# Kernel tuning notes

Measured on AMD Instinct MI355X. Metric: run time of the kernel, lower is better.

## Reference

```python
import jax, jax.numpy as jnp
import numpy as np

N_NODES = 100000
N_EDGES = 1600000
F_IN = 128
DIM = 64
N_CLASSES = 40


def setup_inputs() -> dict:
    key = jax.random.key(0)
    ks = jax.random.split(key, 12)
    x = jax.random.normal(ks[0], (N_NODES, F_IN), dtype=jnp.float32)
    edge_index = jax.random.randint(ks[1], (2, N_EDGES), 0, N_NODES, dtype=jnp.int64)
    s = lambda fan_in: 1.0 / np.sqrt(fan_in)
    W1 = jax.random.uniform(ks[2], (F_IN, DIM), jnp.float32, -s(F_IN), s(F_IN))
    b1 = jax.random.uniform(ks[3], (DIM,), jnp.float32, -s(F_IN), s(F_IN))
    W2 = jax.random.uniform(ks[4], (DIM, DIM), jnp.float32, -s(DIM), s(DIM))
    b2 = jax.random.uniform(ks[5], (DIM,), jnp.float32, -s(DIM), s(DIM))
    Wf1 = jax.random.uniform(ks[6], (DIM, DIM), jnp.float32, -s(DIM), s(DIM))
    bf1 = jax.random.uniform(ks[7], (DIM,), jnp.float32, -s(DIM), s(DIM))
    Wf2 = jax.random.uniform(ks[8], (DIM, N_CLASSES), jnp.float32, -s(DIM), s(DIM))
    bf2 = jax.random.uniform(ks[9], (N_CLASSES,), jnp.float32, -s(DIM), s(DIM))
    return {"x": x, "edge_index": edge_index, "W1": W1, "b1": b1,
            "W2": W2, "b2": b2, "Wf1": Wf1, "bf1": bf1, "Wf2": Wf2, "bf2": bf2}


def _gin_agg(h, src, dst, n_nodes):
    # sum_{j in N(i)} h_j : gather along src, scatter-add to dst
    return jax.ops.segment_sum(h[src], dst, num_segments=n_nodes)


def reference(x, edge_index, W1, b1, W2, b2, Wf1, bf1, Wf2, bf2):
    src, dst = edge_index[0], edge_index[1]
    n = x.shape[0]
    # GINConv(Linear), eps=0: Linear(x + sum_neighbors)
    h = jax.nn.relu((x + _gin_agg(x, src, dst, n)) @ W1 + b1)
    h = jax.nn.relu((h + _gin_agg(h, src, dst, n)) @ W2 + b2)
    h = jax.nn.relu(h @ Wf1 + bf1)  # dropout p=0.5 is identity at inference
    logits = h @ Wf2 + bf2
    return jax.nn.log_softmax(logits, axis=1)
```

## Files before the change

kernel.cpp:

```cpp
#include <hip/hip_runtime.h>

#define NN 100000
#define NE 1600000
#define F_IN 128
#define DIM 64
#define NC 40
#define NB 196
#define MAXBE 10240

typedef unsigned short ushort_t;
typedef __attribute__((ext_vector_type(8))) short bf16x8;
typedef __attribute__((ext_vector_type(4))) float f32x4;

static __device__ __forceinline__ float b2f(ushort_t u) {
  return __uint_as_float(((unsigned)u) << 16);
}
static __device__ __forceinline__ ushort_t f2b(float f) {
  unsigned x = __float_as_uint(f);
  return (ushort_t)((x + 0x7fffu + ((x >> 16) & 1u)) >> 16);
}
static __device__ __forceinline__ unsigned pack2(float a, float b) {
  return (unsigned)f2b(a) | ((unsigned)f2b(b) << 16);
}

__global__ __launch_bounds__(256) void k_prep(const float* __restrict__ W1,
                                              const float* __restrict__ W2,
                                              const float* __restrict__ Wf1,
                                              const float* __restrict__ Wf2,
                                              ushort_t* __restrict__ W1T,
                                              ushort_t* __restrict__ W2T,
                                              ushort_t* __restrict__ Wf1T,
                                              ushort_t* __restrict__ Wf2T,
                                              int* __restrict__ bcur) {
  int t = threadIdx.x;
  if (t < NB) bcur[t] = 0;
  for (int i = t; i < 64 * 128; i += 256) { int c = i >> 7, k = i & 127; W1T[i] = f2b(W1[k * 64 + c]); }
  for (int i = t; i < 64 * 64; i += 256)  { int c = i >> 6, k = i & 63;  W2T[i] = f2b(W2[k * 64 + c]); }
  for (int i = t; i < 64 * 64; i += 256)  { int c = i >> 6, k = i & 63;  Wf1T[i] = f2b(Wf1[k * 64 + c]); }
  for (int i = t; i < 48 * 64; i += 256)  { int c = i >> 6, k = i & 63;  Wf2T[i] = (c < NC) ? f2b(Wf2[k * NC + c]) : (ushort_t)0; }
}

__global__ __launch_bounds__(256) void k_part(const int* __restrict__ src,
                                              const int* __restrict__ dst,
                                              int* __restrict__ bcur,
                                              unsigned* __restrict__ part) {
  __shared__ int hist[NB];
  __shared__ int gbase[NB];
  int t = threadIdx.x;
  for (int i = t; i < NB; i += 256) hist[i] = 0;
  __syncthreads();
  int e0 = blockIdx.x * 4096;
  int s[16], dd[16], r[16];
#pragma unroll
  for (int i = 0; i < 16; ++i) {
    int e = e0 + i * 256 + t;
    if (e < NE) {
      dd[i] = dst[e];
      s[i] = src[e];
      r[i] = atomicAdd(&hist[dd[i] >> 9], 1);
    }
  }
  __syncthreads();
  for (int i = t; i < NB; i += 256)
    gbase[i] = hist[i] ? atomicAdd(&bcur[i], hist[i]) : 0;
  __syncthreads();
#pragma unroll
  for (int i = 0; i < 16; ++i) {
    int e = e0 + i * 256 + t;
    if (e < NE) {
      int b = dd[i] >> 9;
      part[(size_t)b * MAXBE + gbase[b] + r[i]] = ((unsigned)(dd[i] & 511) << 17) | (unsigned)s[i];
    }
  }
}

__global__ __launch_bounds__(256) void k_csr(const int* __restrict__ bcur,
                                             const unsigned* __restrict__ part,
                                             int* __restrict__ cnt,
                                             int* __restrict__ offs,
                                             int* __restrict__ slots) {
  __shared__ unsigned pb[MAXBE];
  __shared__ ushort_t rk[MAXBE];
  __shared__ int lcnt[512], loff[512];
  int b = blockIdx.x, t = threadIdx.x;
  int start = b * MAXBE;
  int m = bcur[b];
  if (m > MAXBE) m = MAXBE;
  lcnt[t] = 0; lcnt[t + 256] = 0;
  __syncthreads();
  for (int i = t; i < m; i += 256) {
    unsigned v = part[start + i];
    pb[i] = v;
    rk[i] = (ushort_t)atomicAdd(&lcnt[v >> 17], 1);
  }
  __syncthreads();
  int o0 = lcnt[t], o1 = lcnt[t + 256];
  __syncthreads();
  for (int off = 1; off < 512; off <<= 1) {
    int v0 = (t >= off) ? lcnt[t - off] : 0;
    int v1 = (t + 256 >= off) ? lcnt[t + 256 - off] : 0;
    __syncthreads();
    lcnt[t] += v0;
    lcnt[t + 256] += v1;
    __syncthreads();
  }
  loff[t] = lcnt[t] - o0;
  loff[t + 256] = lcnt[t + 256] - o1;
  int node0 = b << 9;
  if (node0 + t < NN)       { cnt[node0 + t] = o0;       offs[node0 + t] = start + loff[t]; }
  if (node0 + t + 256 < NN) { cnt[node0 + t + 256] = o1; offs[node0 + t + 256] = start + loff[t + 256]; }
  __syncthreads();
  for (int i = t; i < m; i += 256) {
    unsigned v = pb[i];
    slots[start + loff[v >> 17] + rk[i]] = (int)(v & 0x1FFFFu);
  }
}

__global__ __launch_bounds__(256) void k_agg(const ushort_t* __restrict__ yb,
                                             const int* __restrict__ cnt,
                                             const int* __restrict__ offs,
                                             const int* __restrict__ slots,
                                             const float* __restrict__ bias,
                                             ushort_t* __restrict__ hb) {
  int wv = threadIdx.x >> 6, l = threadIdx.x & 63;
  int h = l >> 5;
  int n = blockIdx.x * 8 + wv * 2 + h;
  int li = l & 31;
  int g = (l >> 3) & 3;
  int q = l & 7;
  int cb = q * 16;
  int deg = cnt[n], start = offs[n];
  deg = deg > 64 ? 64 : deg;
  int sv0 = (li < deg) ? slots[start + li] : 0;
  int sv1 = (32 + li < deg) ? slots[start + 32 + li] : 0;
  int dego = __shfl_xor(deg, 32);
  int degmax = deg > dego ? deg : dego;
  float acc[8];
#pragma unroll
  for (int i = 0; i < 8; ++i) acc[i] = 0.f;
  const char* ybp = (const char*)yb;
  int hbase = h << 5;
  for (int j = 0; j < degmax; j += 16) {
    int i0 = j + g, i1 = j + 4 + g, i2 = j + 8 + g, i3 = j + 12 + g;
    int sa, sb, sc, sd;
    if (j < 32) {
      sa = __shfl(sv0, hbase + i0); sb = __shfl(sv0, hbase + i1);
      sc = __shfl(sv0, hbase + i2); sd = __shfl(sv0, hbase + i3);
    } else {
      sa = __shfl(sv1, hbase + (i0 & 31)); sb = __shfl(sv1, hbase + (i1 & 31));
      sc = __shfl(sv1, hbase + (i2 & 31)); sd = __shfl(sv1, hbase + (i3 & 31));
    }
    uint4 u0 = {0,0,0,0}, u1 = {0,0,0,0}, u2 = {0,0,0,0}, u3 = {0,0,0,0};
    if (i0 < deg) u0 = *(const uint4*)(ybp + (size_t)sa * 128 + cb);
    if (i1 < deg) u1 = *(const uint4*)(ybp + (size_t)sb * 128 + cb);
    if (i2 < deg) u2 = *(const uint4*)(ybp + (size_t)sc * 128 + cb);
    if (i3 < deg) u3 = *(const uint4*)(ybp + (size_t)sd * 128 + cb);
    acc[0] += __uint_as_float(u0.x << 16);  acc[1] += __uint_as_float(u0.x & 0xffff0000u);
    acc[2] += __uint_as_float(u0.y << 16);  acc[3] += __uint_as_float(u0.y & 0xffff0000u);
    acc[4] += __uint_as_float(u0.z << 16);  acc[5] += __uint_as_float(u0.z & 0xffff0000u);
    acc[6] += __uint_as_float(u0.w << 16);  acc[7] += __uint_as_float(u0.w & 0xffff0000u);
    acc[0] += __uint_as_float(u1.x << 16);  acc[1] += __uint_as_float(u1.x & 0xffff0000u);
    acc[2] += __uint_as_float(u1.y << 16);  acc[3] += __uint_as_float(u1.y & 0xffff0000u);
    acc[4] += __uint_as_float(u1.z << 16);  acc[5] += __uint_as_float(u1.z & 0xffff0000u);
    acc[6] += __uint_as_float(u1.w << 16);  acc[7] += __uint_as_float(u1.w & 0xffff0000u);
    acc[0] += __uint_as_float(u2.x << 16);  acc[1] += __uint_as_float(u2.x & 0xffff0000u);
    acc[2] += __uint_as_float(u2.y << 16);  acc[3] += __uint_as_float(u2.y & 0xffff0000u);
    acc[4] += __uint_as_float(u2.z << 16);  acc[5] += __uint_as_float(u2.z & 0xffff0000u);
    acc[6] += __uint_as_float(u2.w << 16);  acc[7] += __uint_as_float(u2.w & 0xffff0000u);
    acc[0] += __uint_as_float(u3.x << 16);  acc[1] += __uint_as_float(u3.x & 0xffff0000u);
    acc[2] += __uint_as_float(u3.y << 16);  acc[3] += __uint_as_float(u3.y & 0xffff0000u);
    acc[4] += __uint_as_float(u3.z << 16);  acc[5] += __uint_as_float(u3.z & 0xffff0000u);
    acc[6] += __uint_as_float(u3.w << 16);  acc[7] += __uint_as_float(u3.w & 0xffff0000u);
  }
#pragma unroll
  for (int i = 0; i < 8; ++i) {
    acc[i] += __shfl_xor(acc[i], 8);
    acc[i] += __shfl_xor(acc[i], 16);
  }
  if (li < 8) {
    uint4 yr = *(const uint4*)&yb[(size_t)n * 64 + q * 8];
    float4 ba = *(const float4*)&bias[q * 8];
    float4 bb = *(const float4*)&bias[q * 8 + 4];
    float v0 = fmaxf(__uint_as_float(yr.x << 16)         + acc[0] + ba.x, 0.f);
    float v1 = fmaxf(__uint_as_float(yr.x & 0xffff0000u) + acc[1] + ba.y, 0.f);
    float v2 = fmaxf(__uint_as_float(yr.y << 16)         + acc[2] + ba.z, 0.f);
    float v3 = fmaxf(__uint_as_float(yr.y & 0xffff0000u) + acc[3] + ba.w, 0.f);
    float v4 = fmaxf(__uint_as_float(yr.z << 16)         + acc[4] + bb.x, 0.f);
    float v5 = fmaxf(__uint_as_float(yr.z & 0xffff0000u) + acc[5] + bb.y, 0.f);
    float v6 = fmaxf(__uint_as_float(yr.w << 16)         + acc[6] + bb.z, 0.f);
    float v7 = fmaxf(__uint_as_float(yr.w & 0xffff0000u) + acc[7] + bb.w, 0.f);
    uint4 st;
    st.x = pack2(v0, v1);
    st.y = pack2(v2, v3);
    st.z = pack2(v4, v5);
    st.w = pack2(v6, v7);
    *(uint4*)&hb[(size_t)n * 64 + q * 8] = st;
  }
}

__global__ __launch_bounds__(256) void k_gemm1(const float* __restrict__ x,
                                               const ushort_t* __restrict__ W1T,
                                               ushort_t* __restrict__ yb) {
  __shared__ ushort_t H[64 * 136];
  int t = threadIdx.x, w = t >> 6, l = t & 63;
  int g = l >> 4, r16 = l & 15;
  int node0 = blockIdx.x * 64;
  bf16x8 B[4][4];
#pragma unroll
  for (int nt = 0; nt < 4; ++nt)
#pragma unroll
    for (int kt = 0; kt < 4; ++kt)
      B[nt][kt] = *(const bf16x8*)&W1T[(16 * nt + r16) * 128 + 32 * kt + 8 * g];
#pragma unroll
  for (int j = 0; j < 8; ++j) {
    int f = t + 256 * j;
    int e = f * 4;
    int n = e >> 7, c = e & 127;
    int gn = node0 + n; if (gn >= NN) gn = NN - 1;
    float4 v = *(const float4*)&x[(size_t)gn * 128 + c];
    ushort4 pv;
    pv.x = f2b(v.x); pv.y = f2b(v.y); pv.z = f2b(v.z); pv.w = f2b(v.w);
    *(ushort4*)&H[n * 136 + c] = pv;
  }
  __syncthreads();
  f32x4 acc[4] = {{0.f,0.f,0.f,0.f},{0.f,0.f,0.f,0.f},{0.f,0.f,0.f,0.f},{0.f,0.f,0.f,0.f}};
#pragma unroll
  for (int kt = 0; kt < 4; ++kt) {
    bf16x8 A = *(const bf16x8*)&H[(16 * w + r16) * 136 + 32 * kt + 8 * g];
#pragma unroll
    for (int nt = 0; nt < 4; ++nt)
      acc[nt] = __builtin_amdgcn_mfma_f32_16x16x32_bf16(A, B[nt][kt], acc[nt], 0, 0, 0);
  }
#pragma unroll
  for (int nt = 0; nt < 4; ++nt)
#pragma unroll
    for (int i = 0; i < 4; ++i) {
      int node = node0 + 16 * w + 4 * g + i;
      if (node < NN)
        yb[(size_t)node * 64 + 16 * nt + r16] = f2b(acc[nt][i]);
    }
}

__global__ __launch_bounds__(256) void k_mid(const ushort_t* __restrict__ hb,
                                             const ushort_t* __restrict__ W2T,
                                             ushort_t* __restrict__ yb) {
  __shared__ ushort_t H[64 * 72];
  int t = threadIdx.x, w = t >> 6, l = t & 63;
  int g = l >> 4, r16 = l & 15;
  int node0 = blockIdx.x * 64;
  bf16x8 B[4][2];
#pragma unroll
  for (int nt = 0; nt < 4; ++nt)
#pragma unroll
    for (int kt = 0; kt < 2; ++kt)
      B[nt][kt] = *(const bf16x8*)&W2T[(16 * nt + r16) * 64 + 32 * kt + 8 * g];
#pragma unroll
  for (int j = 0; j < 2; ++j) {
    int i = t + 256 * j;
    int n = i >> 3, c8 = (i & 7) * 8;
    int gn = node0 + n; if (gn >= NN) gn = NN - 1;
    uint4 u = *(const uint4*)&hb[(size_t)gn * 64 + c8];
    *(uint4*)&H[n * 72 + c8] = u;
  }
  __syncthreads();
  f32x4 acc[4] = {{0.f,0.f,0.f,0.f},{0.f,0.f,0.f,0.f},{0.f,0.f,0.f,0.f},{0.f,0.f,0.f,0.f}};
#pragma unroll
  for (int kt = 0; kt < 2; ++kt) {
    bf16x8 A = *(const bf16x8*)&H[(16 * w + r16) * 72 + 32 * kt + 8 * g];
#pragma unroll
    for (int nt = 0; nt < 4; ++nt)
      acc[nt] = __builtin_amdgcn_mfma_f32_16x16x32_bf16(A, B[nt][kt], acc[nt], 0, 0, 0);
  }
#pragma unroll
  for (int nt = 0; nt < 4; ++nt)
#pragma unroll
    for (int i = 0; i < 4; ++i) {
      int node = node0 + 16 * w + 4 * g + i;
      if (node < NN)
        yb[(size_t)node * 64 + 16 * nt + r16] = f2b(acc[nt][i]);
    }
}

__global__ __launch_bounds__(256) void k_final(const ushort_t* __restrict__ hb,
                                               const ushort_t* __restrict__ Wf1T,
                                               const float* __restrict__ bf1,
                                               const ushort_t* __restrict__ Wf2T,
                                               const float* __restrict__ bf2,
                                               float* __restrict__ out) {
  __shared__ ushort_t H[64 * 72];
  __shared__ ushort_t H2[64 * 72];
  int t = threadIdx.x, w = t >> 6, l = t & 63;
  int g = l >> 4, r16 = l & 15;
  int node0 = blockIdx.x * 64;
  bf16x8 B1[4][2], B2[3][2];
#pragma unroll
  for (int nt = 0; nt < 4; ++nt)
#pragma unroll
    for (int kt = 0; kt < 2; ++kt)
      B1[nt][kt] = *(const bf16x8*)&Wf1T[(16 * nt + r16) * 64 + 32 * kt + 8 * g];
#pragma unroll
  for (int nt = 0; nt < 3; ++nt)
#pragma unroll
    for (int kt = 0; kt < 2; ++kt)
      B2[nt][kt] = *(const bf16x8*)&Wf2T[(16 * nt + r16) * 64 + 32 * kt + 8 * g];
#pragma unroll
  for (int j = 0; j < 2; ++j) {
    int i = t + 256 * j;
    int n = i >> 3, c8 = (i & 7) * 8;
    int gn = node0 + n; if (gn >= NN) gn = NN - 1;
    uint4 u = *(const uint4*)&hb[(size_t)gn * 64 + c8];
    *(uint4*)&H[n * 72 + c8] = u;
  }
  __syncthreads();
  f32x4 acc[4] = {{0.f,0.f,0.f,0.f},{0.f,0.f,0.f,0.f},{0.f,0.f,0.f,0.f},{0.f,0.f,0.f,0.f}};
#pragma unroll
  for (int kt = 0; kt < 2; ++kt) {
    bf16x8 A = *(const bf16x8*)&H[(16 * w + r16) * 72 + 32 * kt + 8 * g];
#pragma unroll
    for (int nt = 0; nt < 4; ++nt)
      acc[nt] = __builtin_amdgcn_mfma_f32_16x16x32_bf16(A, B1[nt][kt], acc[nt], 0, 0, 0);
  }
#pragma unroll
  for (int nt = 0; nt < 4; ++nt) {
    float bias = bf1[16 * nt + r16];
#pragma unroll
    for (int i = 0; i < 4; ++i) {
      float v = fmaxf(acc[nt][i] + bias, 0.f);
      H2[(16 * w + 4 * g + i) * 72 + 16 * nt + r16] = f2b(v);
    }
  }
  __syncthreads();
  f32x4 acc2[3] = {{0.f,0.f,0.f,0.f},{0.f,0.f,0.f,0.f},{0.f,0.f,0.f,0.f}};
#pragma unroll
  for (int kt = 0; kt < 2; ++kt) {
    bf16x8 A2 = *(const bf16x8*)&H2[(16 * w + r16) * 72 + 32 * kt + 8 * g];
#pragma unroll
    for (int nt = 0; nt < 3; ++nt)
      acc2[nt] = __builtin_amdgcn_mfma_f32_16x16x32_bf16(A2, B2[nt][kt], acc2[nt], 0, 0, 0);
  }
  float lg[3][4];
#pragma unroll
  for (int nt = 0; nt < 3; ++nt) {
    int col = 16 * nt + r16;
    float bias = (col < NC) ? bf2[col] : 0.f;
#pragma unroll
    for (int i = 0; i < 4; ++i)
      lg[nt][i] = (col < NC) ? acc2[nt][i] + bias : -1e30f;
  }
#pragma unroll
  for (int i = 0; i < 4; ++i) {
    float m = fmaxf(fmaxf(lg[0][i], lg[1][i]), lg[2][i]);
#pragma unroll
    for (int off = 1; off < 16; off <<= 1) m = fmaxf(m, __shfl_xor(m, off));
    float s = 0.f;
#pragma unroll
    for (int nt = 0; nt < 3; ++nt)
      s += (lg[nt][i] > -1e29f) ? __expf(lg[nt][i] - m) : 0.f;
#pragma unroll
    for (int off = 1; off < 16; off <<= 1) s += __shfl_xor(s, off);
    float ls = __logf(s);
    int node = node0 + 16 * w + 4 * g + i;
#pragma unroll
    for (int nt = 0; nt < 3; ++nt) {
      int col = 16 * nt + r16;
      if (col < NC && node < NN)
        out[(size_t)node * NC + col] = lg[nt][i] - m - ls;
    }
  }
}

extern "C" void kernel_launch(void* const* d_in, const int* in_sizes, int n_in,
                              void* d_out, int out_size, void* d_ws, size_t ws_size,
                              hipStream_t stream) {
  const float* x   = (const float*)d_in[0];
  const int*   ei  = (const int*)d_in[1];
  const float* W1  = (const float*)d_in[2];
  const float* b1  = (const float*)d_in[3];
  const float* W2  = (const float*)d_in[4];
  const float* b2  = (const float*)d_in[5];
  const float* Wf1 = (const float*)d_in[6];
  const float* bf1 = (const float*)d_in[7];
  const float* Wf2 = (const float*)d_in[8];
  const float* bf2 = (const float*)d_in[9];
  float* out = (float*)d_out;

  char* ws = (char*)d_ws;
  size_t o = 0;
  int* bcur  = (int*)(ws + o); o += 4096;
  int* cnt   = (int*)(ws + o); o += 400000;
  int* offs  = (int*)(ws + o); o += 400000;
  o = (o + 255) & ~(size_t)255;
  ushort_t* W1T  = (ushort_t*)(ws + o); o += 64 * 128 * 2;
  ushort_t* W2T  = (ushort_t*)(ws + o); o += 64 * 64 * 2;
  ushort_t* Wf1T = (ushort_t*)(ws + o); o += 64 * 64 * 2;
  ushort_t* Wf2T = (ushort_t*)(ws + o); o += 48 * 64 * 2;
  o = (o + 255) & ~(size_t)255;
  unsigned* part = (unsigned*)(ws + o); o += (size_t)NB * MAXBE * 4;
  int* slots = (int*)(ws + o); o += (size_t)NB * MAXBE * 4;
  ushort_t* yb = (ushort_t*)(ws + o); o += (size_t)NN * DIM * 2;
  ushort_t* hb = (ushort_t*)(ws + o); o += (size_t)NN * DIM * 2;

  const int* srcp = ei;
  const int* dstp = ei + NE;

  k_prep<<<1, 256, 0, stream>>>(W1, W2, Wf1, Wf2, W1T, W2T, Wf1T, Wf2T, bcur);
  k_part<<<(NE + 4095) / 4096, 256, 0, stream>>>(srcp, dstp, bcur, part);
  k_csr<<<NB, 256, 0, stream>>>(bcur, part, cnt, offs, slots);
  k_gemm1<<<(NN + 63) / 64, 256, 0, stream>>>(x, W1T, yb);
  k_agg<<<NN / 8, 256, 0, stream>>>(yb, cnt, offs, slots, b1, hb);
  k_mid<<<(NN + 63) / 64, 256, 0, stream>>>(hb, W2T, yb);
  k_agg<<<NN / 8, 256, 0, stream>>>(yb, cnt, offs, slots, b2, hb);
  k_final<<<(NN + 63) / 64, 256, 0, stream>>>(hb, Wf1T, bf1, Wf2T, bf2, out);
}
```

Baseline: 168.4 us.

## Fuse neighbor aggregation into the following GEMM kernels via shared memory

```diff
diff --git a/kernel.cpp b/kernel.cpp
--- a/kernel.cpp
+++ b/kernel.cpp
@@ -116,20 +116,60 @@
   }
 }
 
-__global__ __launch_bounds__(256) void k_agg(const ushort_t* __restrict__ yb,
-                                             const int* __restrict__ cnt,
-                                             const int* __restrict__ offs,
-                                             const int* __restrict__ slots,
-                                             const float* __restrict__ bias,
-                                             ushort_t* __restrict__ hb) {
-  int wv = threadIdx.x >> 6, l = threadIdx.x & 63;
-  int h = l >> 5;
-  int n = blockIdx.x * 8 + wv * 2 + h;
-  int li = l & 31;
-  int g = (l >> 3) & 3;
-  int q = l & 7;
+__global__ __launch_bounds__(256) void k_gemm1(const float* __restrict__ x,
+                                               const ushort_t* __restrict__ W1T,
+                                               ushort_t* __restrict__ yb) {
+  __shared__ ushort_t H[64 * 136];
+  int t = threadIdx.x, w = t >> 6, l = t & 63;
+  int g = l >> 4, r16 = l & 15;
+  int node0 = blockIdx.x * 64;
+  bf16x8 B[4][4];
+#pragma unroll
+  for (int nt = 0; nt < 4; ++nt)
+#pragma unroll
+    for (int kt = 0; kt < 4; ++kt)
+      B[nt][kt] = *(const bf16x8*)&W1T[(16 * nt + r16) * 128 + 32 * kt + 8 * g];
+#pragma unroll
+  for (int j = 0; j < 8; ++j) {
+    int f = t + 256 * j;
+    int e = f * 4;
+    int n = e >> 7, c = e & 127;
+    int gn = node0 + n; if (gn >= NN) gn = NN - 1;
+    float4 v = *(const float4*)&x[(size_t)gn * 128 + c];
+    ushort4 pv;
+    pv.x = f2b(v.x); pv.y = f2b(v.y); pv.z = f2b(v.z); pv.w = f2b(v.w);
+    *(ushort4*)&H[n * 136 + c] = pv;
+  }
+  __syncthreads();
+  f32x4 acc[4] = {{0.f,0.f,0.f,0.f},{0.f,0.f,0.f,0.f},{0.f,0.f,0.f,0.f},{0.f,0.f,0.f,0.f}};
+#pragma unroll
+  for (int kt = 0; kt < 4; ++kt) {
+    bf16x8 A = *(const bf16x8*)&H[(16 * w + r16) * 136 + 32 * kt + 8 * g];
+#pragma unroll
+    for (int nt = 0; nt < 4; ++nt)
+      acc[nt] = __builtin_amdgcn_mfma_f32_16x16x32_bf16(A, B[nt][kt], acc[nt], 0, 0, 0);
+  }
+#pragma unroll
+  for (int nt = 0; nt < 4; ++nt)
+#pragma unroll
+    for (int i = 0; i < 4; ++i) {
+      int node = node0 + 16 * w + 4 * g + i;
+      if (node < NN)
+        yb[(size_t)node * 64 + 16 * nt + r16] = f2b(acc[nt][i]);
+    }
+}
+
+static __device__ __forceinline__ void agg_round(const ushort_t* __restrict__ yb,
+                                                 const int* __restrict__ cnt,
+                                                 const int* __restrict__ offs,
+                                                 const int* __restrict__ slots,
+                                                 const float* __restrict__ bias,
+                                                 ushort_t* __restrict__ H,
+                                                 int n, int nl,
+                                                 int li, int ag, int q, int h) {
   int cb = q * 16;
-  int deg = cnt[n], start = offs[n];
+  int deg = 0, start = 0;
+  if (n < NN) { deg = cnt[n]; start = offs[n]; }
   deg = deg > 64 ? 64 : deg;
   int sv0 = (li < deg) ? slots[start + li] : 0;
   int sv1 = (32 + li < deg) ? slots[start + 32 + li] : 0;
@@ -141,7 +181,7 @@
   const char* ybp = (const char*)yb;
   int hbase = h << 5;
   for (int j = 0; j < degmax; j += 16) {
-    int i0 = j + g, i1 = j + 4 + g, i2 = j + 8 + g, i3 = j + 12 + g;
+    int i0 = j + ag, i1 = j + 4 + ag, i2 = j + 8 + ag, i3 = j + 12 + ag;
     int sa, sb, sc, sd;
     if (j < 32) {
       sa = __shfl(sv0, hbase + i0); sb = __shfl(sv0, hbase + i1);
@@ -177,7 +217,7 @@
     acc[i] += __shfl_xor(acc[i], 8);
     acc[i] += __shfl_xor(acc[i], 16);
   }
-  if (li < 8) {
+  if (li < 8 && n < NN) {
     uint4 yr = *(const uint4*)&yb[(size_t)n * 64 + q * 8];
     float4 ba = *(const float4*)&bias[q * 8];
     float4 bb = *(const float4*)&bias[q * 8 + 4];
@@ -194,39 +234,37 @@
     st.y = pack2(v2, v3);
     st.z = pack2(v4, v5);
     st.w = pack2(v6, v7);
-    *(uint4*)&hb[(size_t)n * 64 + q * 8] = st;
-  }
-}
-
-__global__ __launch_bounds__(256) void k_gemm1(const float* __restrict__ x,
-                                               const ushort_t* __restrict__ W1T,
-                                               ushort_t* __restrict__ yb) {
-  __shared__ ushort_t H[64 * 136];
+    *(uint4*)&H[nl * 72 + q * 8] = st;
+  }
+}
+
+__global__ __launch_bounds__(256) void k_aggmid(const ushort_t* __restrict__ yb,
+                                                const int* __restrict__ cnt,
+                                                const int* __restrict__ offs,
+                                                const int* __restrict__ slots,
+                                                const float* __restrict__ b1,
+                                                const ushort_t* __restrict__ W2T,
+                                                ushort_t* __restrict__ yb2) {
+  __shared__ ushort_t H[64 * 72];
   int t = threadIdx.x, w = t >> 6, l = t & 63;
-  int g = l >> 4, r16 = l & 15;
+  int h = l >> 5, li = l & 31, ag = (l >> 3) & 3, q = l & 7;
   int node0 = blockIdx.x * 64;
-  bf16x8 B[4][4];
+  for (int r = 0; r < 8; ++r) {
+    int nl = w * 16 + r * 2 + h;
+    agg_round(yb, cnt, offs, slots, b1, H, node0 + nl, nl, li, ag, q, h);
+  }
+  __syncthreads();
+  int mg = l >> 4, r16 = l & 15;
+  bf16x8 B[4][2];
 #pragma unroll
   for (int nt = 0; nt < 4; ++nt)
 #pragma unroll
-    for (int kt = 0; kt < 4; ++kt)
-      B[nt][kt] = *(const bf16x8*)&W1T[(16 * nt + r16) * 128 + 32 * kt + 8 * g];
-#pragma unroll
-  for (int j = 0; j < 8; ++j) {
-    int f = t + 256 * j;
-    int e = f * 4;
-    int n = e >> 7, c = e & 127;
-    int gn = node0 + n; if (gn >= NN) gn = NN - 1;
-    float4 v = *(const float4*)&x[(size_t)gn * 128 + c];
-    ushort4 pv;
-    pv.x = f2b(v.x); pv.y = f2b(v.y); pv.z = f2b(v.z); pv.w = f2b(v.w);
-    *(ushort4*)&H[n * 136 + c] = pv;
-  }
-  __syncthreads();
+    for (int kt = 0; kt < 2; ++kt)
+      B[nt][kt] = *(const bf16x8*)&W2T[(16 * nt + r16) * 64 + 32 * kt + 8 * mg];
   f32x4 acc[4] = {{0.f,0.f,0.f,0.f},{0.f,0.f,0.f,0.f},{0.f,0.f,0.f,0.f},{0.f,0.f,0.f,0.f}};
 #pragma unroll
-  for (int kt = 0; kt < 4; ++kt) {
-    bf16x8 A = *(const bf16x8*)&H[(16 * w + r16) * 136 + 32 * kt + 8 * g];
+  for (int kt = 0; kt < 2; ++kt) {
+    bf16x8 A = *(const bf16x8*)&H[(16 * w + r16) * 72 + 32 * kt + 8 * mg];
 #pragma unroll
     for (int nt = 0; nt < 4; ++nt)
       acc[nt] = __builtin_amdgcn_mfma_f32_16x16x32_bf16(A, B[nt][kt], acc[nt], 0, 0, 0);
@@ -235,87 +273,48 @@
   for (int nt = 0; nt < 4; ++nt)
 #pragma unroll
     for (int i = 0; i < 4; ++i) {
-      int node = node0 + 16 * w + 4 * g + i;
+      int node = node0 + 16 * w + 4 * mg + i;
       if (node < NN)
-        yb[(size_t)node * 64 + 16 * nt + r16] = f2b(acc[nt][i]);
-    }
-}
-
-__global__ __launch_bounds__(256) void k_mid(const ushort_t* __restrict__ hb,
-                                             const ushort_t* __restrict__ W2T,
-                                             ushort_t* __restrict__ yb) {
-  __shared__ ushort_t H[64 * 72];
-  int t = threadIdx.x, w = t >> 6, l = t & 63;
-  int g = l >> 4, r16 = l & 15;
-  int node0 = blockIdx.x * 64;
-  bf16x8 B[4][2];
-#pragma unroll
-  for (int nt = 0; nt < 4; ++nt)
-#pragma unroll
-    for (int kt = 0; kt < 2; ++kt)
-      B[nt][kt] = *(const bf16x8*)&W2T[(16 * nt + r16) * 64 + 32 * kt + 8 * g];
-#pragma unroll
-  for (int j = 0; j < 2; ++j) {
-    int i = t + 256 * j;
-    int n = i >> 3, c8 = (i & 7) * 8;
-    int gn = node0 + n; if (gn >= NN) gn = NN - 1;
-    uint4 u = *(const uint4*)&hb[(size_t)gn * 64 + c8];
-    *(uint4*)&H[n * 72 + c8] = u;
-  }
-  __syncthreads();
-  f32x4 acc[4] = {{0.f,0.f,0.f,0.f},{0.f,0.f,0.f,0.f},{0.f,0.f,0.f,0.f},{0.f,0.f,0.f,0.f}};
-#pragma unroll
-  for (int kt = 0; kt < 2; ++kt) {
-    bf16x8 A = *(const bf16x8*)&H[(16 * w + r16) * 72 + 32 * kt + 8 * g];
-#pragma unroll
-    for (int nt = 0; nt < 4; ++nt)
-      acc[nt] = __builtin_amdgcn_mfma_f32_16x16x32_bf16(A, B[nt][kt], acc[nt], 0, 0, 0);
-  }
-#pragma unroll
-  for (int nt = 0; nt < 4; ++nt)
-#pragma unroll
-    for (int i = 0; i < 4; ++i) {
-      int node = node0 + 16 * w + 4 * g + i;
-      if (node < NN)
-        yb[(size_t)node * 64 + 16 * nt + r16] = f2b(acc[nt][i]);
-    }
-}
-
-__global__ __launch_bounds__(256) void k_final(const ushort_t* __restrict__ hb,
-                                               const ushort_t* __restrict__ Wf1T,
-                                               const float* __restrict__ bf1,
-                                               const ushort_t* __restrict__ Wf2T,
-                                               const float* __restrict__ bf2,
-                                               float* __restrict__ out) {
+        yb2[(size_t)node * 64 + 16 * nt + r16] = f2b(acc[nt][i]);
+    }
+}
+
+__global__ __launch_bounds__(256) void k_aggfin(const ushort_t* __restrict__ yb2,
+                                                const int* __restrict__ cnt,
+                                                const int* __restrict__ offs,
+                                                const int* __restrict__ slots,
+                                                const float* __restrict__ b2,
+                                                const ushort_t* __restrict__ Wf1T,
+                                                const float* __restrict__ bf1,
+                                                const ushort_t* __restrict__ Wf2T,
+                                                const float* __restrict__ bf2,
+                                                float* __restrict__ out) {
   __shared__ ushort_t H[64 * 72];
   __shared__ ushort_t H2[64 * 72];
   int t = threadIdx.x, w = t >> 6, l = t & 63;
-  int g = l >> 4, r16 = l & 15;
+  int h = l >> 5, li = l & 31, ag = (l >> 3) & 3, q = l & 7;
   int node0 = blockIdx.x * 64;
+  for (int r = 0; r < 8; ++r) {
+    int nl = w * 16 + r * 2 + h;
+    agg_round(yb2, cnt, offs, slots, b2, H, node0 + nl, nl, li, ag, q, h);
+  }
+  __syncthreads();
+  int mg = l >> 4, r16 = l & 15;
   bf16x8 B1[4][2], B2[3][2];
 #pragma unroll
   for (int nt = 0; nt < 4; ++nt)
 #pragma unroll
     for (int kt = 0; kt < 2; ++kt)
-      B1[nt][kt] = *(const bf16x8*)&Wf1T[(16 * nt + r16) * 64 + 32 * kt + 8 * g];
+      B1[nt][kt] = *(const bf16x8*)&Wf1T[(16 * nt + r16) * 64 + 32 * kt + 8 * mg];
 #pragma unroll
   for (int nt = 0; nt < 3; ++nt)
 #pragma unroll
     for (int kt = 0; kt < 2; ++kt)
-      B2[nt][kt] = *(const bf16x8*)&Wf2T[(16 * nt + r16) * 64 + 32 * kt + 8 * g];
-#pragma unroll
-  for (int j = 0; j < 2; ++j) {
-    int i = t + 256 * j;
-    int n = i >> 3, c8 = (i & 7) * 8;
-    int gn = node0 + n; if (gn >= NN) gn = NN - 1;
-    uint4 u = *(const uint4*)&hb[(size_t)gn * 64 + c8];
-    *(uint4*)&H[n * 72 + c8] = u;
-  }
-  __syncthreads();
+      B2[nt][kt] = *(const bf16x8*)&Wf2T[(16 * nt + r16) * 64 + 32 * kt + 8 * mg];
   f32x4 acc[4] = {{0.f,0.f,0.f,0.f},{0.f,0.f,0.f,0.f},{0.f,0.f,0.f,0.f},{0.f,0.f,0.f,0.f}};
 #pragma unroll
   for (int kt = 0; kt < 2; ++kt) {
-    bf16x8 A = *(const bf16x8*)&H[(16 * w + r16) * 72 + 32 * kt + 8 * g];
+    bf16x8 A = *(const bf16x8*)&H[(16 * w + r16) * 72 + 32 * kt + 8 * mg];
 #pragma unroll
     for (int nt = 0; nt < 4; ++nt)
       acc[nt] = __builtin_amdgcn_mfma_f32_16x16x32_bf16(A, B1[nt][kt], acc[nt], 0, 0, 0);
@@ -326,14 +325,14 @@
 #pragma unroll
     for (int i = 0; i < 4; ++i) {
       float v = fmaxf(acc[nt][i] + bias, 0.f);
-      H2[(16 * w + 4 * g + i) * 72 + 16 * nt + r16] = f2b(v);
+      H2[(16 * w + 4 * mg + i) * 72 + 16 * nt + r16] = f2b(v);
     }
   }
   __syncthreads();
   f32x4 acc2[3] = {{0.f,0.f,0.f,0.f},{0.f,0.f,0.f,0.f},{0.f,0.f,0.f,0.f}};
 #pragma unroll
   for (int kt = 0; kt < 2; ++kt) {
-    bf16x8 A2 = *(const bf16x8*)&H2[(16 * w + r16) * 72 + 32 * kt + 8 * g];
+    bf16x8 A2 = *(const bf16x8*)&H2[(16 * w + r16) * 72 + 32 * kt + 8 * mg];
 #pragma unroll
     for (int nt = 0; nt < 3; ++nt)
       acc2[nt] = __builtin_amdgcn_mfma_f32_16x16x32_bf16(A2, B2[nt][kt], acc2[nt], 0, 0, 0);
@@ -359,7 +358,7 @@
 #pragma unroll
     for (int off = 1; off < 16; off <<= 1) s += __shfl_xor(s, off);
     float ls = __logf(s);
-    int node = node0 + 16 * w + 4 * g + i;
+    int node = node0 + 16 * w + 4 * mg + i;
 #pragma unroll
     for (int nt = 0; nt < 3; ++nt) {
       int col = 16 * nt + r16;
@@ -397,8 +396,8 @@
   o = (o + 255) & ~(size_t)255;
   unsigned* part = (unsigned*)(ws + o); o += (size_t)NB * MAXBE * 4;
   int* slots = (int*)(ws + o); o += (size_t)NB * MAXBE * 4;
-  ushort_t* yb = (ushort_t*)(ws + o); o += (size_t)NN * DIM * 2;
-  ushort_t* hb = (ushort_t*)(ws + o); o += (size_t)NN * DIM * 2;
+  ushort_t* yb  = (ushort_t*)(ws + o); o += (size_t)NN * DIM * 2;
+  ushort_t* yb2 = (ushort_t*)(ws + o); o += (size_t)NN * DIM * 2;
 
   const int* srcp = ei;
   const int* dstp = ei + NE;
@@ -407,8 +406,6 @@
   k_part<<<(NE + 4095) / 4096, 256, 0, stream>>>(srcp, dstp, bcur, part);
   k_csr<<<NB, 256, 0, stream>>>(bcur, part, cnt, offs, slots);
   k_gemm1<<<(NN + 63) / 64, 256, 0, stream>>>(x, W1T, yb);
-  k_agg<<<NN / 8, 256, 0, stream>>>(yb, cnt, offs, slots, b1, hb);
-  k_mid<<<(NN + 63) / 64, 256, 0, stream>>>(hb, W2T, yb);
-  k_agg<<<NN / 8, 256, 0, stream>>>(yb, cnt, offs, slots, b2, hb);
-  k_final<<<(NN + 63) / 64, 256, 0, stream>>>(hb, Wf1T, bf1, Wf2T, bf2, out);
-}
+  k_aggmid<<<(NN + 63) / 64, 256, 0, stream>>>(yb, cnt, offs, slots, b1, W2T, yb2);
+  k_aggfin<<<(NN + 63) / 64, 256, 0, stream>>>(yb2, cnt, offs, slots, b2, Wf1T, bf1, Wf2T, bf2, out);
+}
```

Measured after the change: 178.3 us. 5.8% more time.
